# Kernel tuning notes

Measured on AMD Instinct MI355X. Metric: run time of the kernel, lower is better.

## Reference

```python
import jax, jax.numpy as jnp
import numpy as np

N_NODES = 100000
N_EDGES = 1600000
NUM_FEATURES = 128
HIDDEN = 64
NUM_CLASSES = 2


def _gcn_norm(edge_index, num_nodes):
    # PyG gcn_norm: add self-loops, symmetric degree normalization.
    loop = jnp.arange(num_nodes, dtype=edge_index.dtype)
    src = jnp.concatenate([edge_index[0], loop])
    dst = jnp.concatenate([edge_index[1], loop])
    deg = jax.ops.segment_sum(jnp.ones_like(src, dtype=jnp.float32), dst,
                              num_segments=num_nodes)
    dinv = jnp.where(deg > 0, jax.lax.rsqrt(deg), 0.0)
    norm = dinv[src] * dinv[dst]  # [E + N]
    return src, dst, norm


def _gcn_conv(x, src, dst, norm, W, b, num_nodes):
    h = x @ W  # linear transform first (PyG GCNConv)
    msg = h[src] * norm[:, None]  # gather + edge scaling, [E+N, H]
    out = jax.ops.segment_sum(msg, dst, num_segments=num_nodes)  # scatter-add
    return out + b


def setup_inputs() -> dict:
    key = jax.random.key(0)
    ks = jax.random.split(key, 8)
    x = jax.random.normal(ks[0], (N_NODES, NUM_FEATURES), dtype=jnp.float32)
    edge_index = jax.random.randint(ks[1], (2, N_EDGES), 0, N_NODES, dtype=jnp.int32)
    def glorot(k, shape):
        lim = np.sqrt(6.0 / (shape[0] + shape[1]))
        return jax.random.uniform(k, shape, jnp.float32, -lim, lim)
    return {
        "x": x,
        "edge_index": edge_index,
        "W1": glorot(ks[2], (NUM_FEATURES, HIDDEN)),
        "b1": jnp.zeros((HIDDEN,), jnp.float32),
        "W2": glorot(ks[3], (HIDDEN, HIDDEN)),
        "b2": jnp.zeros((HIDDEN,), jnp.float32),
        "W3": glorot(ks[4], (HIDDEN, HIDDEN)),
        "b3": jnp.zeros((HIDDEN,), jnp.float32),
        "Wlin": glorot(ks[5], (HIDDEN, NUM_CLASSES)),
        "blin": jnp.zeros((NUM_CLASSES,), jnp.float32),
    }


def reference(x, edge_index, W1, b1, W2, b2, W3, b3, Wlin, blin):
    num_nodes = x.shape[0]
    src, dst, norm = _gcn_norm(edge_index, num_nodes)
    # eval mode: dropout is identity
    h = jax.nn.relu(_gcn_conv(x, src, dst, norm, W1, b1, num_nodes))
    h = jax.nn.relu(_gcn_conv(h, src, dst, norm, W2, b2, num_nodes))
    h = jax.nn.relu(_gcn_conv(h, src, dst, norm, W3, b3, num_nodes))
    logits = h @ Wlin + blin
    return jax.nn.log_softmax(logits, axis=1)
```

## Files before the change

kernel.cpp:

```cpp
#include <hip/hip_runtime.h>
#include <cstdint>
#include <cstddef>

#define NF 128
#define NH 64


__global__ __launch_bounds__(256) void count_kernel(const int* __restrict__ ei, int E,
                                                    int* __restrict__ cnt, int RW) {
  int pass = blockIdx.x & 7;
  int i = (blockIdx.x >> 3) * 256 + threadIdx.x;
  if (i * 4 >= E) return;
  int4 d = ((const int4*)(ei + E))[i];
  int lo = pass * RW, hi = lo + RW;
  if (d.x >= lo && d.x < hi) atomicAdd(&cnt[d.x], 1);
  if (d.y >= lo && d.y < hi) atomicAdd(&cnt[d.y], 1);
  if (d.z >= lo && d.z < hi) atomicAdd(&cnt[d.z], 1);
  if (d.w >= lo && d.w < hi) atomicAdd(&cnt[d.w], 1);
}

__global__ __launch_bounds__(256) void partial_kernel(const int* __restrict__ cnt, int N,
                                                      int* __restrict__ part) {
  __shared__ int sd[256];
  int t = threadIdx.x;
  int idx = blockIdx.x * 1024 + t * 4;
  int s = 0;
#pragma unroll
  for (int j = 0; j < 4; ++j)
    if (idx + j < N) s += cnt[idx + j];
  sd[t] = s;
  __syncthreads();
  for (int off = 128; off > 0; off >>= 1) {
    if (t < off) sd[t] += sd[t + off];
    __syncthreads();
  }
  if (t == 0) part[blockIdx.x] = sd[0];
}

__global__ __launch_bounds__(128) void scanp_kernel(int* __restrict__ part, int NB,
                                                    int* __restrict__ rowptrN) {
  __shared__ int s[128];
  int t = threadIdx.x;
  int v = (t < NB) ? part[t] : 0;
  s[t] = v;
  __syncthreads();
  for (int off = 1; off < 128; off <<= 1) {
    int add = (t >= off) ? s[t - off] : 0;
    __syncthreads();
    s[t] += add;
    __syncthreads();
  }
  if (t < NB) part[t] = s[t] - v;
  if (t == 0) rowptrN[0] = s[127];
}

__global__ __launch_bounds__(256) void rowptr_kernel(const int* __restrict__ cnt,
                                                     const int* __restrict__ part,
                                                     int* __restrict__ rowptr,
                                                     int* __restrict__ cnt2,
                                                     float* __restrict__ dinv, int N) {
  __shared__ int s[256];
  int t = threadIdx.x;
  int idx = blockIdx.x * 1024 + t * 4;
  int c[4];
  int ts = 0;
#pragma unroll
  for (int j = 0; j < 4; ++j) {
    c[j] = (idx + j < N) ? cnt[idx + j] : 0;
    ts += c[j];
  }
  s[t] = ts;
  __syncthreads();
  for (int off = 1; off < 256; off <<= 1) {
    int add = (t >= off) ? s[t - off] : 0;
    __syncthreads();
    s[t] += add;
    __syncthreads();
  }
  int run = s[t] - ts + part[blockIdx.x];
#pragma unroll
  for (int j = 0; j < 4; ++j) {
    if (idx + j < N) {
      rowptr[idx + j] = run;
      cnt2[idx + j] = run;
      dinv[idx + j] = rsqrtf((float)(c[j] + 1));
    }
    run += c[j];
  }
}

__global__ __launch_bounds__(256) void fill_kernel(const int* __restrict__ ei, int E,
                                                   int* __restrict__ cnt2,
                                                   const float* __restrict__ dinv,
                                                   int2* __restrict__ col2, int RW) {
  int pass = blockIdx.x & 7;
  int i = (blockIdx.x >> 3) * 256 + threadIdx.x;
  if (i * 4 >= E) return;
  int4 sv = ((const int4*)ei)[i];
  int4 dv = ((const int4*)(ei + E))[i];
  int lo = pass * RW, hi = lo + RW;
  int ss[4] = {sv.x, sv.y, sv.z, sv.w};
  int dd[4] = {dv.x, dv.y, dv.z, dv.w};
#pragma unroll
  for (int j = 0; j < 4; ++j) {
    int d = dd[j];
    if (d < lo || d >= hi) continue;
    int s = ss[j];
    float w = dinv[s] * dinv[d];
    int pos = atomicAdd(&cnt2[d], 1);
    col2[pos] = make_int2(s, __float_as_int(w));
  }
}


template <int K>
__global__ __launch_bounds__(256, 4) void gemm_kernel(const float* __restrict__ X,
                                                      const float* __restrict__ W,
                                                      float* __restrict__ H, int N) {
  __shared__ float XsT[64][68];
  __shared__ float Ws[64 * 64];
  const int tid = threadIdx.x;
  const int n0 = blockIdx.x * 64;
  const int tn = (tid >> 4) * 4;
  const int tf = (tid & 15) * 4;

  float acc[4][4];
#pragma unroll
  for (int i = 0; i < 4; ++i)
#pragma unroll
    for (int j = 0; j < 4; ++j) acc[i][j] = 0.f;

  for (int kt = 0; kt < K / 64; ++kt) {
    {
      const float4* Wg = (const float4*)(W + (size_t)kt * 64 * 64);
      float4* Wl = (float4*)Ws;
#pragma unroll
      for (int j = 0; j < 4; ++j) Wl[tid + j * 256] = Wg[tid + j * 256];
    }
#pragma unroll
    for (int j = 0; j < 4; ++j) {
      int idx = tid + j * 256;
      int n = idx >> 4;
      int kq = idx & 15;
      float4 v = make_float4(0.f, 0.f, 0.f, 0.f);
      if (n0 + n < N)
        v = *(const float4*)(X + (size_t)(n0 + n) * K + kt * 64 + kq * 4);
      XsT[kq * 4 + 0][n] = v.x;
      XsT[kq * 4 + 1][n] = v.y;
      XsT[kq * 4 + 2][n] = v.z;
      XsT[kq * 4 + 3][n] = v.w;
    }
    __syncthreads();
#pragma unroll 8
    for (int k = 0; k < 64; ++k) {
      float4 xv = *(const float4*)(&XsT[k][tn]);
      float4 wv = *(const float4*)(&Ws[k * 64 + tf]);
      acc[0][0] = fmaf(xv.x, wv.x, acc[0][0]);
      acc[0][1] = fmaf(xv.x, wv.y, acc[0][1]);
      acc[0][2] = fmaf(xv.x, wv.z, acc[0][2]);
      acc[0][3] = fmaf(xv.x, wv.w, acc[0][3]);
      acc[1][0] = fmaf(xv.y, wv.x, acc[1][0]);
      acc[1][1] = fmaf(xv.y, wv.y, acc[1][1]);
      acc[1][2] = fmaf(xv.y, wv.z, acc[1][2]);
      acc[1][3] = fmaf(xv.y, wv.w, acc[1][3]);
      acc[2][0] = fmaf(xv.z, wv.x, acc[2][0]);
      acc[2][1] = fmaf(xv.z, wv.y, acc[2][1]);
      acc[2][2] = fmaf(xv.z, wv.z, acc[2][2]);
      acc[2][3] = fmaf(xv.z, wv.w, acc[2][3]);
      acc[3][0] = fmaf(xv.w, wv.x, acc[3][0]);
      acc[3][1] = fmaf(xv.w, wv.y, acc[3][1]);
      acc[3][2] = fmaf(xv.w, wv.z, acc[3][2]);
      acc[3][3] = fmaf(xv.w, wv.w, acc[3][3]);
    }
    __syncthreads();
  }
#pragma unroll
  for (int i = 0; i < 4; ++i) {
    int n = n0 + tn + i;
    if (n < N)
      *(float4*)(H + (size_t)n * 64 + tf) =
          make_float4(acc[i][0], acc[i][1], acc[i][2], acc[i][3]);
  }
}

template <int FINAL>
__global__ __launch_bounds__(256) void prop_fused_kernel(
    const float* __restrict__ H, const int* __restrict__ rowptr,
    const int2* __restrict__ col2, const float* __restrict__ dinv,
    const float* __restrict__ bias, const float* __restrict__ Wn,
    const float* __restrict__ blin, float* __restrict__ out, int N) {
  __shared__ float Ws[64 * 64];
  __shared__ float rbuf[4][64];
  const int lane = threadIdx.x & 63;
  const int widx = threadIdx.x >> 6;

  if (!FINAL) {
    const float4* Wg = (const float4*)Wn;
    float4* Wl = (float4*)Ws;
    for (int i = threadIdx.x; i < 1024; i += 256) Wl[i] = Wg[i];
    __syncthreads();
  }

  int n = blockIdx.x * 4 + widx;
  n = __builtin_amdgcn_readfirstlane(n);
  if (n >= N) return;

  float wl0 = 0.f, wl1 = 0.f, bl0 = 0.f, bl1 = 0.f;
  if (FINAL) {
    wl0 = Wn[lane * 2 + 0];
    wl1 = Wn[lane * 2 + 1];
    bl0 = blin[0];
    bl1 = blin[1];
  }

  int e0 = rowptr[n];
  int e1 = rowptr[n + 1];
  float di = dinv[n];
  const int2* ec = col2 + e0;
  const int m = e1 - e0;

  float acc0 = H[(size_t)n * 64 + lane] * (di * di);
  float acc1 = 0.f;

  int sC[8], sN[8];
  float wC[8], wN[8];
  const int nfull = m >> 3;

#define LOADC(S, W, base)                           \
  {                                                 \
    _Pragma("unroll") for (int j = 0; j < 8; ++j) { \
      int2 c = ec[(base) + j];                      \
      S[j] = c.x;                                   \
      W[j] = __int_as_float(c.y);                   \
    }                                               \
  }

  if (nfull > 0) LOADC(sC, wC, 0)
  for (int b = 0; b < nfull; ++b) {
    float h[8];
#pragma unroll
    for (int j = 0; j < 8; ++j) h[j] = H[(size_t)sC[j] * 64 + lane];
    if (b + 1 < nfull) LOADC(sN, wN, (b + 1) * 8)
#pragma unroll
    for (int j = 0; j < 8; ++j) {
      if (j & 1)
        acc1 = fmaf(wC[j], h[j], acc1);
      else
        acc0 = fmaf(wC[j], h[j], acc0);
    }
#pragma unroll
    for (int j = 0; j < 8; ++j) {
      sC[j] = sN[j];
      wC[j] = wN[j];
    }
  }
#undef LOADC
  for (int t = nfull * 8; t < m; ++t) {
    int2 c = ec[t];
    acc0 = fmaf(__int_as_float(c.y), H[(size_t)c.x * 64 + lane], acc0);
  }
  float r = acc0 + acc1 + bias[lane];
  r = r > 0.f ? r : 0.f;

  if (FINAL) {
    float t0 = r * wl0;
    float t1 = r * wl1;
#pragma unroll
    for (int off = 32; off > 0; off >>= 1) {
      t0 += __shfl_xor(t0, off, 64);
      t1 += __shfl_xor(t1, off, 64);
    }
    if (lane == 0) {
      float l0 = t0 + bl0;
      float l1 = t1 + bl1;
      float mx = fmaxf(l0, l1);
      float lz = mx + logf(expf(l0 - mx) + expf(l1 - mx));
      out[(size_t)n * 2 + 0] = l0 - lz;
      out[(size_t)n * 2 + 1] = l1 - lz;
    }
  } else {
    rbuf[widx][lane] = r;
    __builtin_amdgcn_wave_barrier();
    float o = 0.f;
#pragma unroll
    for (int q = 0; q < 16; ++q) {
      float4 rv = *(const float4*)(&rbuf[widx][4 * q]);
      o = fmaf(rv.x, Ws[(4 * q + 0) * 64 + lane], o);
      o = fmaf(rv.y, Ws[(4 * q + 1) * 64 + lane], o);
      o = fmaf(rv.z, Ws[(4 * q + 2) * 64 + lane], o);
      o = fmaf(rv.w, Ws[(4 * q + 3) * 64 + lane], o);
    }
    out[(size_t)n * 64 + lane] = o;
  }
}


extern "C" void kernel_launch(void* const* d_in, const int* in_sizes, int n_in,
                              void* d_out, int out_size, void* d_ws, size_t ws_size,
                              hipStream_t stream) {
  const float* x  = (const float*)d_in[0];
  const int*   ei = (const int*)d_in[1];
  const float* W1 = (const float*)d_in[2];
  const float* b1 = (const float*)d_in[3];
  const float* W2 = (const float*)d_in[4];
  const float* b2 = (const float*)d_in[5];
  const float* W3 = (const float*)d_in[6];
  const float* b3 = (const float*)d_in[7];
  const float* Wl = (const float*)d_in[8];
  const float* bl = (const float*)d_in[9];
  float* out = (float*)d_out;

  const int N = in_sizes[0] / NF;
  const int E = in_sizes[1] / 2;

  char* w = (char*)d_ws;
  size_t off = 0;
  auto alloc = [&](size_t bytes) {
    void* p = w + off;
    off += bytes;
    off = (off + 15) & ~(size_t)15;
    return p;
  };
  int*   cnt    = (int*)alloc((size_t)N * 4);
  int*   cnt2   = (int*)alloc((size_t)N * 4);
  int*   rowptr = (int*)alloc((size_t)(N + 1) * 4);
  int*   part   = (int*)alloc(256 * 4);
  float* dinv   = (float*)alloc((size_t)N * 4);
  int2*  col2   = (int2*)alloc((size_t)E * 8);
  float* hA     = (float*)alloc((size_t)N * NH * 4);
  float* hB     = (float*)alloc((size_t)N * NH * 4);

  const int NB = (N + 1023) / 1024;
  const int RW = (N + 7) / 8;
  const int NCHUNK = (E / 4 + 255) / 256;

  hipMemsetAsync(cnt, 0, (size_t)N * 4, stream);
  hipLaunchKernelGGL(count_kernel, dim3(8 * NCHUNK), dim3(256), 0, stream,
                     ei, E, cnt, RW);
  hipLaunchKernelGGL(partial_kernel, dim3(NB), dim3(256), 0, stream, cnt, N, part);
  hipLaunchKernelGGL(scanp_kernel, dim3(1), dim3(128), 0, stream, part, NB, rowptr + N);
  hipLaunchKernelGGL(rowptr_kernel, dim3(NB), dim3(256), 0, stream,
                     cnt, part, rowptr, cnt2, dinv, N);
  hipLaunchKernelGGL(fill_kernel, dim3(8 * NCHUNK), dim3(256), 0, stream,
                     ei, E, cnt2, dinv, col2, RW);

  hipLaunchKernelGGL(gemm_kernel<128>, dim3((N + 63) / 64), dim3(256), 0, stream, x, W1, hA, N);
  hipLaunchKernelGGL(prop_fused_kernel<0>, dim3((N + 3) / 4), dim3(256), 0, stream,
                     hA, rowptr, col2, dinv, b1, W2, (const float*)nullptr, hB, N);
  hipLaunchKernelGGL(prop_fused_kernel<0>, dim3((N + 3) / 4), dim3(256), 0, stream,
                     hB, rowptr, col2, dinv, b2, W3, (const float*)nullptr, hA, N);
  hipLaunchKernelGGL(prop_fused_kernel<1>, dim3((N + 3) / 4), dim3(256), 0, stream,
                     hA, rowptr, col2, dinv, b3, Wl, bl, out, N);
}
```

Baseline: 459.8 us.

## Store hidden features in bf16 and split wave into two edge streams

Intermediate node features are stored as packed bf16 pairs instead of fp32, which halves the bytes gathered per neighbor in the three propagation kernels. Each wave now handles two edges at once: each half-wave processes alternating edges with 32 lanes covering two features each, and the halves are combined with a cross-lane shuffle. This targets the random-gather bandwidth that dominates the sparse aggregation. In exchange, the intermediates lose precision, and the old software prefetch of the next edge batch is dropped.

```diff
diff --git a/kernel.cpp b/kernel.cpp
--- a/kernel.cpp
+++ b/kernel.cpp
@@ -4,6 +4,15 @@
 
 #define NF 128
 #define NH 64
+
+typedef unsigned int uint32;
+
+__device__ inline unsigned short f2bf(float f) {
+  unsigned int u = __float_as_uint(f);
+  return (unsigned short)((u + 0x7FFF + ((u >> 16) & 1)) >> 16);
+}
+__device__ inline float bf2f_lo(uint32 u) { return __uint_as_float(u << 16); }
+__device__ inline float bf2f_hi(uint32 u) { return __uint_as_float(u & 0xFFFF0000u); }
 
 
 __global__ __launch_bounds__(256) void count_kernel(const int* __restrict__ ei, int E,
@@ -116,7 +125,7 @@
 template <int K>
 __global__ __launch_bounds__(256, 4) void gemm_kernel(const float* __restrict__ X,
                                                       const float* __restrict__ W,
-                                                      float* __restrict__ H, int N) {
+                                                      uint32* __restrict__ Hb, int N) {
   __shared__ float XsT[64][68];
   __shared__ float Ws[64 * 64];
   const int tid = threadIdx.x;
@@ -177,22 +186,26 @@
 #pragma unroll
   for (int i = 0; i < 4; ++i) {
     int n = n0 + tn + i;
-    if (n < N)
-      *(float4*)(H + (size_t)n * 64 + tf) =
-          make_float4(acc[i][0], acc[i][1], acc[i][2], acc[i][3]);
+    if (n < N) {
+      uint32 p0 = (uint32)f2bf(acc[i][0]) | ((uint32)f2bf(acc[i][1]) << 16);
+      uint32 p1 = (uint32)f2bf(acc[i][2]) | ((uint32)f2bf(acc[i][3]) << 16);
+      *(uint2*)(Hb + (size_t)n * 32 + tf / 2) = make_uint2(p0, p1);
+    }
   }
 }
 
 template <int FINAL>
 __global__ __launch_bounds__(256) void prop_fused_kernel(
-    const float* __restrict__ H, const int* __restrict__ rowptr,
+    const uint32* __restrict__ H32, const int* __restrict__ rowptr,
     const int2* __restrict__ col2, const float* __restrict__ dinv,
     const float* __restrict__ bias, const float* __restrict__ Wn,
-    const float* __restrict__ blin, float* __restrict__ out, int N) {
+    const float* __restrict__ blin, void* __restrict__ outv, int N) {
   __shared__ float Ws[64 * 64];
   __shared__ float rbuf[4][64];
   const int lane = threadIdx.x & 63;
   const int widx = threadIdx.x >> 6;
+  const int fl = lane & 31;
+  const int half = lane >> 5;
 
   if (!FINAL) {
     const float4* Wg = (const float4*)Wn;
@@ -204,14 +217,6 @@
   int n = blockIdx.x * 4 + widx;
   n = __builtin_amdgcn_readfirstlane(n);
   if (n >= N) return;
-
-  float wl0 = 0.f, wl1 = 0.f, bl0 = 0.f, bl1 = 0.f;
-  if (FINAL) {
-    wl0 = Wn[lane * 2 + 0];
-    wl1 = Wn[lane * 2 + 1];
-    bl0 = blin[0];
-    bl1 = blin[1];
-  }
 
   int e0 = rowptr[n];
   int e1 = rowptr[n + 1];
@@ -219,67 +224,79 @@
   const int2* ec = col2 + e0;
   const int m = e1 - e0;
 
-  float acc0 = H[(size_t)n * 64 + lane] * (di * di);
-  float acc1 = 0.f;
-
-  int sC[8], sN[8];
-  float wC[8], wN[8];
-  const int nfull = m >> 3;
-
-#define LOADC(S, W, base)                           \
-  {                                                 \
-    _Pragma("unroll") for (int j = 0; j < 8; ++j) { \
-      int2 c = ec[(base) + j];                      \
-      S[j] = c.x;                                   \
-      W[j] = __int_as_float(c.y);                   \
-    }                                               \
-  }
-
-  if (nfull > 0) LOADC(sC, wC, 0)
+  float acc0 = 0.f, acc1 = 0.f;
+  if (half == 0) {
+    uint32 u = H32[(size_t)n * 32 + fl];
+    float w = di * di;
+    acc0 = bf2f_lo(u) * w;
+    acc1 = bf2f_hi(u) * w;
+  }
+
+  const int npair = m >> 1;
+  const int nfull = npair >> 3;
   for (int b = 0; b < nfull; ++b) {
-    float h[8];
-#pragma unroll
-    for (int j = 0; j < 8; ++j) h[j] = H[(size_t)sC[j] * 64 + lane];
-    if (b + 1 < nfull) LOADC(sN, wN, (b + 1) * 8)
+    int s[8];
+    float wv[8];
 #pragma unroll
     for (int j = 0; j < 8; ++j) {
-      if (j & 1)
-        acc1 = fmaf(wC[j], h[j], acc1);
-      else
-        acc0 = fmaf(wC[j], h[j], acc0);
-    }
+      int2 c = ec[2 * (b * 8 + j) + half];
+      s[j] = c.x;
+      wv[j] = __int_as_float(c.y);
+    }
+    uint32 u[8];
+#pragma unroll
+    for (int j = 0; j < 8; ++j) u[j] = H32[(size_t)s[j] * 32 + fl];
 #pragma unroll
     for (int j = 0; j < 8; ++j) {
-      sC[j] = sN[j];
-      wC[j] = wN[j];
-    }
-  }
-#undef LOADC
-  for (int t = nfull * 8; t < m; ++t) {
-    int2 c = ec[t];
-    acc0 = fmaf(__int_as_float(c.y), H[(size_t)c.x * 64 + lane], acc0);
-  }
-  float r = acc0 + acc1 + bias[lane];
-  r = r > 0.f ? r : 0.f;
+      acc0 = fmaf(wv[j], bf2f_lo(u[j]), acc0);
+      acc1 = fmaf(wv[j], bf2f_hi(u[j]), acc1);
+    }
+  }
+  for (int t = nfull * 8; t < npair; ++t) {
+    int2 c = ec[2 * t + half];
+    uint32 u = H32[(size_t)c.x * 32 + fl];
+    float w = __int_as_float(c.y);
+    acc0 = fmaf(w, bf2f_lo(u), acc0);
+    acc1 = fmaf(w, bf2f_hi(u), acc1);
+  }
+  if ((m & 1) && half == 0) {
+    int2 c = ec[m - 1];
+    uint32 u = H32[(size_t)c.x * 32 + fl];
+    float w = __int_as_float(c.y);
+    acc0 = fmaf(w, bf2f_lo(u), acc0);
+    acc1 = fmaf(w, bf2f_hi(u), acc1);
+  }
+  acc0 += __shfl_xor(acc0, 32, 64);
+  acc1 += __shfl_xor(acc1, 32, 64);
+
+  float2 bv = ((const float2*)bias)[fl];
+  float r0 = acc0 + bv.x;
+  float r1 = acc1 + bv.y;
+  r0 = r0 > 0.f ? r0 : 0.f;
+  r1 = r1 > 0.f ? r1 : 0.f;
 
   if (FINAL) {
-    float t0 = r * wl0;
-    float t1 = r * wl1;
+    float t0 = 0.f, t1 = 0.f;
+    if (half == 0) {
+      t0 = r0 * Wn[4 * fl + 0] + r1 * Wn[4 * fl + 2];
+      t1 = r0 * Wn[4 * fl + 1] + r1 * Wn[4 * fl + 3];
+    }
 #pragma unroll
     for (int off = 32; off > 0; off >>= 1) {
       t0 += __shfl_xor(t0, off, 64);
       t1 += __shfl_xor(t1, off, 64);
     }
     if (lane == 0) {
-      float l0 = t0 + bl0;
-      float l1 = t1 + bl1;
+      float* out = (float*)outv;
+      float l0 = t0 + blin[0];
+      float l1 = t1 + blin[1];
       float mx = fmaxf(l0, l1);
       float lz = mx + logf(expf(l0 - mx) + expf(l1 - mx));
       out[(size_t)n * 2 + 0] = l0 - lz;
       out[(size_t)n * 2 + 1] = l1 - lz;
     }
   } else {
-    rbuf[widx][lane] = r;
+    if (half == 0) *(float2*)(&rbuf[widx][2 * fl]) = make_float2(r0, r1);
     __builtin_amdgcn_wave_barrier();
     float o = 0.f;
 #pragma unroll
@@ -290,7 +307,7 @@
       o = fmaf(rv.z, Ws[(4 * q + 2) * 64 + lane], o);
       o = fmaf(rv.w, Ws[(4 * q + 3) * 64 + lane], o);
     }
-    out[(size_t)n * 64 + lane] = o;
+    ((unsigned short*)outv)[(size_t)n * 64 + lane] = f2bf(o);
   }
 }
 
@@ -321,14 +338,14 @@
     off = (off + 15) & ~(size_t)15;
     return p;
   };
-  int*   cnt    = (int*)alloc((size_t)N * 4);
-  int*   cnt2   = (int*)alloc((size_t)N * 4);
-  int*   rowptr = (int*)alloc((size_t)(N + 1) * 4);
-  int*   part   = (int*)alloc(256 * 4);
-  float* dinv   = (float*)alloc((size_t)N * 4);
-  int2*  col2   = (int2*)alloc((size_t)E * 8);
-  float* hA     = (float*)alloc((size_t)N * NH * 4);
-  float* hB     = (float*)alloc((size_t)N * NH * 4);
+  int*    cnt    = (int*)alloc((size_t)N * 4);
+  int*    cnt2   = (int*)alloc((size_t)N * 4);
+  int*    rowptr = (int*)alloc((size_t)(N + 1) * 4);
+  int*    part   = (int*)alloc(256 * 4);
+  float*  dinv   = (float*)alloc((size_t)N * 4);
+  int2*   col2   = (int2*)alloc((size_t)E * 8);
+  uint32* hA     = (uint32*)alloc((size_t)N * 32 * 4);
+  uint32* hB     = (uint32*)alloc((size_t)N * 32 * 4);
 
   const int NB = (N + 1023) / 1024;
   const int RW = (N + 7) / 8;
@@ -344,11 +361,12 @@
   hipLaunchKernelGGL(fill_kernel, dim3(8 * NCHUNK), dim3(256), 0, stream,
                      ei, E, cnt2, dinv, col2, RW);
 
-  hipLaunchKernelGGL(gemm_kernel<128>, dim3((N + 63) / 64), dim3(256), 0, stream, x, W1, hA, N);
+  hipLaunchKernelGGL(gemm_kernel<128>, dim3((N + 63) / 64), dim3(256), 0, stream,
+                     x, W1, hA, N);
   hipLaunchKernelGGL(prop_fused_kernel<0>, dim3((N + 3) / 4), dim3(256), 0, stream,
-                     hA, rowptr, col2, dinv, b1, W2, (const float*)nullptr, hB, N);
+                     hA, rowptr, col2, dinv, b1, W2, (const float*)nullptr, (void*)hB, N);
   hipLaunchKernelGGL(prop_fused_kernel<0>, dim3((N + 3) / 4), dim3(256), 0, stream,
-                     hB, rowptr, col2, dinv, b2, W3, (const float*)nullptr, hA, N);
+                     hB, rowptr, col2, dinv, b2, W3, (const float*)nullptr, (void*)hA, N);
   hipLaunchKernelGGL(prop_fused_kernel<1>, dim3((N + 3) / 4), dim3(256), 0, stream,
-                     hA, rowptr, col2, dinv, b3, Wl, bl, out, N);
-}
+                     hA, rowptr, col2, dinv, b3, Wl, bl, (void*)out, N);
+}
```

After: 444.9 us. 3.2% less time.
